# Kernel optimization log

Hardware: AMD Instinct MI355X
Metric: run time of the kernel (lower is better)

Reference implementation:

```python
import jax, jax.numpy as jnp
from jax import lax
import numpy as np

B, N = 8, 16384
C = 16            # layer_channels
K = 2             # kernel_size
L = 30            # layer_nums (layer 0 is plain causal conv, 29 gated layers)
AGG = 64          # agregate1x1 out channels
OUT = 256         # output1x1 out channels (8-bit classes)


def causal_conv(x, w, dilation):
    # x: (B, Cin, N), w: (Cout, Cin, K) -> (B, Cout, N), left-padded (causal)
    k = w.shape[-1]
    return lax.conv_general_dilated(
        x, w, window_strides=(1,), padding=[(dilation * (k - 1), 0)],
        rhs_dilation=(dilation,), dimension_numbers=('NCH', 'OIH', 'NCH'))


def setup_inputs() -> dict:
    key = jax.random.key(0)
    ks = jax.random.split(key, 16)
    s = 0.1
    x = jax.random.normal(ks[0], (B, N), dtype=jnp.float32) * 8000.0  # raw 16-bit-ish audio
    lengths = jax.random.randint(ks[1], (B,), N // 2, N, dtype=jnp.int32)
    return {
        'x': x,
        'lengths': lengths,
        'W0': jax.random.normal(ks[2], (C, 1, K), dtype=jnp.float32) * s,
        'b0': jnp.zeros((C,), dtype=jnp.float32),
        'Wf': jax.random.normal(ks[3], (L - 1, C, C, K), dtype=jnp.float32) * s,
        'bf': jnp.zeros((L - 1, C), dtype=jnp.float32),
        'Wg': jax.random.normal(ks[4], (L - 1, C, C, K), dtype=jnp.float32) * s,
        'bg': jnp.zeros((L - 1, C), dtype=jnp.float32),
        'Wr': jax.random.normal(ks[5], (L - 1, C, C), dtype=jnp.float32) * s,
        'br': jnp.zeros((L - 1, C), dtype=jnp.float32),
        'Wa': jax.random.normal(ks[6], (AGG, C), dtype=jnp.float32) * s,
        'ba': jnp.zeros((AGG,), dtype=jnp.float32),
        'Wo': jax.random.normal(ks[7], (OUT, AGG), dtype=jnp.float32) * s,
        'bo': jnp.zeros((OUT,), dtype=jnp.float32),
    }


def reference(x, lengths, W0, b0, Wf, bf, Wg, bg, Wr, br, Wa, ba, Wo, bo):
    inp = (x / 32768.0)[:, None, :]                     # (B,1,N), 65536/2 scaling
    # layer 0: plain causal conv 1 -> C
    h = causal_conv(inp, W0, 1) + b0[:, None]           # (B,C,N)
    skip = h
    inp = inp + h                                       # (B,1,N)+(B,C,N) broadcast
    for i in range(1, L):
        d = 2 ** (i % 10)
        j = i - 1
        f = jnp.tanh(causal_conv(inp, Wf[j], d) + bf[j][:, None])
        g = jax.nn.sigmoid(causal_conv(inp, Wg[j], d) + bg[j][:, None])
        z = f * g                                       # gated activation
        out = jnp.einsum('oc,bcn->bon', Wr[j], z) + br[j][:, None]
        skip = skip + out                               # skip-sum accumulation
        inp = inp + out                                 # residual
    a = jnp.einsum('oc,bcn->bon', Wa, jax.nn.relu(skip)) + ba[:, None]
    o = jnp.einsum('oc,bcn->bon', Wo, jax.nn.relu(a)) + bo[:, None]
    logp = jax.nn.log_softmax(o, axis=1)                # (B,OUT,N)
    mask = (jnp.arange(N) < lengths[:, None])[:, None, :].astype(logp.dtype)
    return logp * mask
```

## Files before the change

kernel.cpp:

```cpp
#include <hip/hip_runtime.h>
#include <hip/hip_bf16.h>

#define NN 16384
#define NC 16
#define NPOSTOT 131072
#define NLAY 29
#define TOUT 256
#define LSTR 24

typedef float4 f4;
typedef short bf16x8 __attribute__((ext_vector_type(8)));
typedef float f32x4 __attribute__((ext_vector_type(4)));

#define OFF_WF 0
#define OFF_WG (NLAY * 512)
#define OFF_WR (2 * NLAY * 512)
#define OFF_WA (3 * NLAY * 512)
#define OFF_WO (3 * NLAY * 512 + 2048)
#define PK_TOT (OFF_WO + 16384)

static __device__ __forceinline__ short to_bf16(float f) {
    __hip_bfloat16 h = __float2bfloat16(f);
    short s;
    __builtin_memcpy(&s, &h, 2);
    return s;
}
static __device__ __forceinline__ float from_bf16(short s) {
    unsigned int u = ((unsigned int)(unsigned short)s) << 16;
    float f;
    __builtin_memcpy(&f, &u, 4);
    return f;
}

__global__ __launch_bounds__(256) void prepack_k(
    const float* __restrict__ Wf, const float* __restrict__ Wg,
    const float* __restrict__ Wr, const float* __restrict__ Wa,
    const float* __restrict__ Wo, short* __restrict__ pk)
{
    const int i = blockIdx.x * 256 + threadIdx.x;
    if (i >= PK_TOT) return;
    float val;
    if (i < OFF_WG) {
        const int j = i >> 9, r = i & 511, l = r >> 3, j8 = r & 7;
        const int o = l & 15, h = l >> 4;
        const int k = h * 8 + j8, tap = k >> 4, c = k & 15;
        val = Wf[((j * 16 + o) * 16 + c) * 2 + tap];
    } else if (i < OFF_WA) {
        const int i2 = i - OFF_WG;
        if (i2 < NLAY * 512) {
            const int j = i2 >> 9, r = i2 & 511, l = r >> 3, j8 = r & 7;
            const int o = l & 15, h = l >> 4;
            const int k = h * 8 + j8, tap = k >> 4, c = k & 15;
            val = Wg[((j * 16 + o) * 16 + c) * 2 + tap];
        } else {
            const int i3 = i2 - NLAY * 512;
            const int j = i3 >> 9, r = i3 & 511, l = r >> 3, j8 = r & 7;
            const int o = l & 15, h = l >> 4;
            val = (j8 < 4) ? Wr[j * 256 + o * 16 + h * 4 + j8] : 0.0f;
        }
    } else if (i < OFF_WO) {
        const int i2 = i - OFF_WA;
        const int mt = i2 >> 9, r = i2 & 511, l = r >> 3, j8 = r & 7;
        const int og = mt * 16 + (l & 15), h = l >> 4;
        const int k = h * 8 + j8;
        val = (k < 16) ? Wa[og * 16 + k] : 0.0f;
    } else {
        const int i2 = i - OFF_WO;
        const int qt = i2 >> 10, hf = (i2 >> 9) & 1, r = i2 & 511;
        const int l = r >> 3, j8 = r & 7;
        const int q = qt * 16 + (l & 15), h = l >> 4;
        const int kg = hf * 32 + (j8 >> 2) * 16 + h * 4 + (j8 & 3);
        val = Wo[q * 64 + kg];
    }
    pk[i] = to_bf16(val);
}

static __device__ __forceinline__ f32x4 gated_core2(
    bf16x8 bx, bf16x8 af_, bf16x8 ag_, bf16x8 ar_,
    f32x4 cf, f32x4 cg, f32x4 cr)
{
    const f32x4 fp = __builtin_amdgcn_mfma_f32_16x16x32_bf16(af_, bx, cf, 0, 0, 0);
    const f32x4 gp = __builtin_amdgcn_mfma_f32_16x16x32_bf16(ag_, bx, cg, 0, 0, 0);

    bf16x8 bz;
#pragma unroll
    for (int r = 0; r < 4; ++r) {
        const float ef = __expf(2.0f * fminf(fp[r], 43.0f));
        const float eg = __expf(-gp[r]);
        const float den = fmaf(ef, eg, ef) + (eg + 1.0f);
        bz[r] = to_bf16((ef - 1.0f) * __builtin_amdgcn_rcpf(den));
        bz[r + 4] = 0;
    }
    return __builtin_amdgcn_mfma_f32_16x16x32_bf16(ar_, bx = bz, cr, 0, 0, 0);
}

struct SegCfg { int d[8]; int nl; int jbase; int H; int l0; };

constexpr SegCfg CFGS[12] = {
    {{2, 4, 8, 16, 32, 64, 0, 0},  6, 0,  128, 1},
    {{128, 0, 0, 0, 0, 0, 0, 0},   1, 6,  0,   0},
    {{256, 0, 0, 0, 0, 0, 0, 0},   1, 7,  0,   0},
    {{512, 1, 2, 4, 8, 16, 32, 0}, 7, 8,  64,  0},
    {{64, 0, 0, 0, 0, 0, 0, 0},    1, 15, 0,   0},
    {{128, 0, 0, 0, 0, 0, 0, 0},   1, 16, 0,   0},
    {{256, 0, 0, 0, 0, 0, 0, 0},   1, 17, 0,   0},
    {{512, 1, 2, 4, 8, 16, 32, 0}, 7, 18, 64,  0},
    {{64, 0, 0, 0, 0, 0, 0, 0},    1, 25, 0,   0},
    {{128, 0, 0, 0, 0, 0, 0, 0},   1, 26, 0,   0},
    {{256, 0, 0, 0, 0, 0, 0, 0},   1, 27, 0,   0},
    {{512, 0, 0, 0, 0, 0, 0, 0},   1, 28, 0,   0},
};

template<int KI>
__global__ __launch_bounds__((TOUT + CFGS[KI].H) * 2)
void fused_t(const short* __restrict__ src, const float* __restrict__ x,
             const float* __restrict__ W0, const float* __restrict__ b0,
             short* __restrict__ dst, const short* __restrict__ pk,
             const float* __restrict__ bfA, const float* __restrict__ bgA,
             const float* __restrict__ brA)
{
    constexpr SegCfg cfg = CFGS[KI];
    constexpr int H = cfg.H;
    constexpr int Wp = TOUT + H;
    constexpr bool MULTI = (cfg.nl > 1);
    constexpr int LDSSZ = MULTI ? 2 * Wp * LSTR : 8;
    __shared__ short lds[LDSSZ];
    short* ldsA = lds;
    short* ldsB = lds + (MULTI ? Wp * LSTR : 0);

    const int t = threadIdx.x, lane = t & 63, wv = t >> 6;
    const int h = lane >> 4, i16 = lane & 15;
    const int tap = h >> 1, c0 = (h & 1) * 8;
    const int pbase = blockIdx.x * TOUT;
    const int bb = pbase >> 14, n0 = pbase & (NN - 1);
    const float* xrow = x + (size_t)bb * NN;
    const short* srow = src + (size_t)bb * NN * NC;

    const int l0r = wv * 32 + i16;
    const int l1r = l0r + 16;
    const int nA = n0 - H + l0r;
    const int nB = nA + 16;

    f32x4 res0, res1;

    {
        constexpr int d = cfg.d[0];
        constexpr int j = cfg.jbase;
        const bf16x8 af = *(const bf16x8*)(pk + OFF_WF + j * 512 + lane * 8);
        const bf16x8 ag = *(const bf16x8*)(pk + OFF_WG + j * 512 + lane * 8);
        const bf16x8 ar = *(const bf16x8*)(pk + OFF_WR + j * 512 + lane * 8);
        const f4 v1 = *(const f4*)(bfA + j * 16 + h * 4);
        const f4 v2 = *(const f4*)(bgA + j * 16 + h * 4);
        const f4 v3 = *(const f4*)(brA + j * 16 + h * 4);
        const f32x4 cf = {v1.x, v1.y, v1.z, v1.w};
        const f32x4 cg = {v2.x, v2.y, v2.z, v2.w};
        const f32x4 cr = {v3.x, v3.y, v3.z, v3.w};

        auto tile0 = [&](int l, int n, f32x4& res) {
            const int ns = tap ? n : n - d;
            bf16x8 bx = {0, 0, 0, 0, 0, 0, 0, 0};
            if (cfg.l0) {
                if (ns >= 0) {
                    const float xs = xrow[ns] * (1.0f / 32768.0f);
                    const float xm = (ns >= 1) ? xrow[ns - 1] * (1.0f / 32768.0f) : 0.0f;
#pragma unroll
                    for (int q2 = 0; q2 < 8; ++q2) {
                        const int c = c0 + q2;
                        bx[q2] = to_bf16(xs + fmaf(W0[c * 2], xm,
                                          fmaf(W0[c * 2 + 1], xs, b0[c])));
                    }
                }
            } else {
                if (ns >= 0) bx = *(const bf16x8*)(srow + (size_t)ns * NC + c0);
            }
            const f32x4 o = gated_core2(bx, af, ag, ar, cf, cg, cr);

            float r0, r1, r2, r3;
            if (cfg.l0) {
                if (n >= 0) {
                    const float xs = xrow[n] * (1.0f / 32768.0f);
                    const float xm = (n >= 1) ? xrow[n - 1] * (1.0f / 32768.0f) : 0.0f;
                    const int c = h * 4;
                    r0 = xs + fmaf(W0[c * 2 + 0], xm, fmaf(W0[c * 2 + 1], xs, b0[c + 0]));
                    r1 = xs + fmaf(W0[c * 2 + 2], xm, fmaf(W0[c * 2 + 3], xs, b0[c + 1]));
                    r2 = xs + fmaf(W0[c * 2 + 4], xm, fmaf(W0[c * 2 + 5], xs, b0[c + 2]));
                    r3 = xs + fmaf(W0[c * 2 + 6], xm, fmaf(W0[c * 2 + 7], xs, b0[c + 3]));
                } else { r0 = r1 = r2 = r3 = 0.0f; }
            } else {
                if (n >= 0) {
                    const short4 ov = *(const short4*)(srow + (size_t)n * NC + h * 4);
                    r0 = from_bf16(ov.x); r1 = from_bf16(ov.y);
                    r2 = from_bf16(ov.z); r3 = from_bf16(ov.w);
                } else { r0 = r1 = r2 = r3 = 0.0f; }
            }
            res[0] = r0 + o[0]; res[1] = r1 + o[1];
            res[2] = r2 + o[2]; res[3] = r3 + o[3];
            if (MULTI) {
                *(short4*)(ldsA + l * LSTR + h * 4) =
                    make_short4(to_bf16(res[0]), to_bf16(res[1]),
                                to_bf16(res[2]), to_bf16(res[3]));
            }
        };
        tile0(l0r, nA, res0);
        tile0(l1r, nB, res1);
    }
    if (MULTI) __syncthreads();

    int cur = 0;
#pragma unroll
    for (int s = 1; s < cfg.nl; ++s) {
        const int d = cfg.d[s];
        const int j = cfg.jbase + s;
        const bf16x8 af = *(const bf16x8*)(pk + OFF_WF + j * 512 + lane * 8);
        const bf16x8 ag = *(const bf16x8*)(pk + OFF_WG + j * 512 + lane * 8);
        const bf16x8 ar = *(const bf16x8*)(pk + OFF_WR + j * 512 + lane * 8);
        const f4 v1 = *(const f4*)(bfA + j * 16 + h * 4);
        const f4 v2 = *(const f4*)(bgA + j * 16 + h * 4);
        const f4 v3 = *(const f4*)(brA + j * 16 + h * 4);
        const f32x4 cf = {v1.x, v1.y, v1.z, v1.w};
        const f32x4 cg = {v2.x, v2.y, v2.z, v2.w};
        const f32x4 cr = {v3.x, v3.y, v3.z, v3.w};
        const short* rb = cur ? ldsB : ldsA;
        short* wb = cur ? ldsA : ldsB;
        const bool wr = (s + 1 < cfg.nl);

        auto tileL = [&](int l, int n, f32x4& res) {
            const int nt = tap ? n : n - d;
            int lt = tap ? l : l - d;
            if (lt < 0) lt = 0;
            bf16x8 bx = {0, 0, 0, 0, 0, 0, 0, 0};
            if (nt >= 0) bx = *(const bf16x8*)(rb + lt * LSTR + c0);
            const f32x4 o = gated_core2(bx, af, ag, ar, cf, cg, cr);
            res[0] += o[0]; res[1] += o[1]; res[2] += o[2]; res[3] += o[3];
            if (wr) {
                *(short4*)(wb + l * LSTR + h * 4) =
                    make_short4(to_bf16(res[0]), to_bf16(res[1]),
                                to_bf16(res[2]), to_bf16(res[3]));
            }
        };
        tileL(l0r, nA, res0);
        tileL(l1r, nB, res1);
        if (s + 1 < cfg.nl) __syncthreads();
        cur ^= 1;
    }

    if (l0r >= H) {
        *(short4*)(dst + ((size_t)bb * NN + nA) * NC + h * 4) =
            make_short4(to_bf16(res0[0]), to_bf16(res0[1]),
                        to_bf16(res0[2]), to_bf16(res0[3]));
    }
    if (l1r >= H) {
        *(short4*)(dst + ((size_t)bb * NN + nB) * NC + h * 4) =
            make_short4(to_bf16(res1[0]), to_bf16(res1[1]),
                        to_bf16(res1[2]), to_bf16(res1[3]));
    }
}

__global__ __launch_bounds__(512, 2) void headm_k(
    const short* __restrict__ fin, const float* __restrict__ x,
    const int* __restrict__ lengths,
    const short* __restrict__ pka, const float* __restrict__ ba,
    const short* __restrict__ pko, const float* __restrict__ bo,
    float* __restrict__ out)
{
    __shared__ short ldsW[16384];

    const int t = threadIdx.x;
    const int lane = t & 63;
    const int wv = t >> 6;
    const int i16 = lane & 15;
    const int h = lane >> 4;
    const int pos = blockIdx.x * 128 + wv * 16 + i16;
    const int b = pos >> 14;
    const int n = pos & (NN - 1);

#pragma unroll
    for (int i = 0; i < 4; ++i)
        ((f4*)ldsW)[t + i * 512] = ((const f4*)pko)[t + i * 512];

    bf16x8 bs;
    if (h < 2) {
        const float xs = x[pos] * (1.0f / 32768.0f);
        const bf16x8 v = *(const bf16x8*)(fin + (size_t)pos * NC + h * 8);
#pragma unroll
        for (int j = 0; j < 8; ++j)
            bs[j] = to_bf16(fmaxf(from_bf16(v[j]) - xs, 0.0f));
    } else {
#pragma unroll
        for (int j = 0; j < 8; ++j) bs[j] = 0;
    }

    float ra[16];
#pragma unroll
    for (int mt = 0; mt < 4; ++mt) {
        const bf16x8 aa = *(const bf16x8*)(pka + (mt * 64 + lane) * 8);
        const f4 bav = *(const f4*)(ba + mt * 16 + h * 4);
        f32x4 c = {bav.x, bav.y, bav.z, bav.w};
        c = __builtin_amdgcn_mfma_f32_16x16x32_bf16(aa, bs, c, 0, 0, 0);
#pragma unroll
        for (int r = 0; r < 4; ++r) ra[mt * 4 + r] = fmaxf(c[r], 0.0f);
    }
    bf16x8 blo, bhi;
#pragma unroll
    for (int j = 0; j < 8; ++j) { blo[j] = to_bf16(ra[j]); bhi[j] = to_bf16(ra[8 + j]); }

    __syncthreads();

    float lg[64];
#pragma unroll
    for (int qt = 0; qt < 16; ++qt) {
        const bf16x8 a0 = *(const bf16x8*)(ldsW + ((qt * 2 + 0) * 64 + lane) * 8);
        const bf16x8 a1 = *(const bf16x8*)(ldsW + ((qt * 2 + 1) * 64 + lane) * 8);
        const f4 bov = *(const f4*)(bo + qt * 16 + h * 4);
        f32x4 c = {bov.x, bov.y, bov.z, bov.w};
        c = __builtin_amdgcn_mfma_f32_16x16x32_bf16(a0, blo, c, 0, 0, 0);
        c = __builtin_amdgcn_mfma_f32_16x16x32_bf16(a1, bhi, c, 0, 0, 0);
#pragma unroll
        for (int r = 0; r < 4; ++r) lg[qt * 4 + r] = c[r];
    }

    float m = lg[0];
#pragma unroll
    for (int j = 1; j < 64; ++j) m = fmaxf(m, lg[j]);
    m = fmaxf(m, __shfl_xor(m, 16, 64));
    m = fmaxf(m, __shfl_xor(m, 32, 64));
    float s = 0.0f;
#pragma unroll
    for (int j = 0; j < 64; ++j) s += __expf(lg[j] - m);
    s += __shfl_xor(s, 16, 64);
    s += __shfl_xor(s, 32, 64);
    const float lse = m + __logf(s);
    const bool valid = n < lengths[b];

    float* ob = out + (size_t)b * 256 * NN + n;
#pragma unroll
    for (int qt = 0; qt < 16; ++qt)
#pragma unroll
        for (int r = 0; r < 4; ++r)
            ob[(size_t)(qt * 16 + h * 4 + r) * NN] = valid ? (lg[qt * 4 + r] - lse) : 0.0f;
}

extern "C" void kernel_launch(void* const* d_in, const int* in_sizes, int n_in,
                              void* d_out, int out_size, void* d_ws, size_t ws_size,
                              hipStream_t stream)
{
    const float* x       = (const float*)d_in[0];
    const int*   lengths = (const int*)d_in[1];
    const float* W0      = (const float*)d_in[2];
    const float* b0      = (const float*)d_in[3];
    const float* Wf      = (const float*)d_in[4];
    const float* bf      = (const float*)d_in[5];
    const float* Wg      = (const float*)d_in[6];
    const float* bg      = (const float*)d_in[7];
    const float* Wr      = (const float*)d_in[8];
    const float* br      = (const float*)d_in[9];
    const float* Wa      = (const float*)d_in[10];
    const float* ba      = (const float*)d_in[11];
    const float* Wo      = (const float*)d_in[12];
    const float* bo      = (const float*)d_in[13];
    float* out = (float*)d_out;

    short* bufA = (short*)d_ws;
    short* bufB = bufA + (size_t)NPOSTOT * NC;
    short* pk   = bufB + (size_t)NPOSTOT * NC;

    prepack_k<<<dim3((PK_TOT + 255) / 256), dim3(256), 0, stream>>>(
        Wf, Wg, Wr, Wa, Wo, pk);

#define FUSED(K, SRC, DST)                                                     \
    fused_t<K><<<dim3(NPOSTOT / TOUT), dim3((TOUT + CFGS[K].H) * 2), 0,        \
                 stream>>>(SRC, x, W0, b0, DST, pk, bf, bg, br)

    FUSED(0,  bufA, bufA);
    FUSED(1,  bufA, bufB);
    FUSED(2,  bufB, bufA);
    FUSED(3,  bufA, bufB);
    FUSED(4,  bufB, bufA);
    FUSED(5,  bufA, bufB);
    FUSED(6,  bufB, bufA);
    FUSED(7,  bufA, bufB);
    FUSED(8,  bufB, bufA);
    FUSED(9,  bufA, bufB);
    FUSED(10, bufB, bufA);
    FUSED(11, bufA, bufB);
#undef FUSED

    headm_k<<<dim3(NPOSTOT / 128), dim3(512), 0, stream>>>(
        bufB, x, lengths, pk + OFF_WA, ba, pk + OFF_WO, bo, out);
}
```

Measured before the change: 143.1 us.

## Switch gated layers to 32x32x16 MFMA with fused filter/gate tile

Replaces the three 16x16x32 MFMAs per tile (filter, gate, residual) with 32x32x16 MFMAs. Filter and gate weights are stacked into one 32-row A matrix, the two taps are split across two MFMAs, and channels are permuted so the accumulator layout lines up with the B operand of the next layer. Each lane now keeps 8 channels of the residual in registers and reuses them as the tap-0 input instead of reloading from LDS. Block size and output tile are retuned per segment: multi-layer segments use 128 outputs and non-multi segments 256. This is meant to cut MFMA count and wasted zero-padding work, at the cost of a more intricate weight-prepack permutation and different occupancy.

```diff
diff --git a/kernel.cpp b/kernel.cpp
--- a/kernel.cpp
+++ b/kernel.cpp
@@ -5,19 +5,22 @@
 #define NC 16
 #define NPOSTOT 131072
 #define NLAY 29
-#define TOUT 256
 #define LSTR 24
 
 typedef float4 f4;
 typedef short bf16x8 __attribute__((ext_vector_type(8)));
 typedef float f32x4 __attribute__((ext_vector_type(4)));
-
-#define OFF_WF 0
-#define OFF_WG (NLAY * 512)
-#define OFF_WR (2 * NLAY * 512)
-#define OFF_WA (3 * NLAY * 512)
-#define OFF_WO (3 * NLAY * 512 + 2048)
+typedef float f32x16 __attribute__((ext_vector_type(16)));
+
+#define OFF_C  0
+#define OFF_R  (NLAY * 1024)
+#define OFF_WA (OFF_R + NLAY * 512)
+#define OFF_WO (OFF_WA + 2048)
 #define PK_TOT (OFF_WO + 16384)
+
+__host__ __device__ constexpr int PERM(int s) {
+    return (s & 3) | ((s & 4) << 1) | ((s & 8) >> 1);
+}
 
 static __device__ __forceinline__ short to_bf16(float f) {
     __hip_bfloat16 h = __float2bfloat16(f);
@@ -40,34 +43,28 @@
     const int i = blockIdx.x * 256 + threadIdx.x;
     if (i >= PK_TOT) return;
     float val;
-    if (i < OFF_WG) {
-        const int j = i >> 9, r = i & 511, l = r >> 3, j8 = r & 7;
-        const int o = l & 15, h = l >> 4;
-        const int k = h * 8 + j8, tap = k >> 4, c = k & 15;
-        val = Wf[((j * 16 + o) * 16 + c) * 2 + tap];
+    if (i < OFF_R) {
+        const int j = i >> 10, r = i & 1023, tp = r >> 9, rr = r & 511;
+        const int l = rr >> 3, j8 = rr & 7;
+        const int row = l & 31, hi = l >> 5;
+        const int c = PERM(hi * 8 + j8);
+        val = (row < 16) ? Wf[((j * 16 + row) * 16 + c) * 2 + tp]
+                         : Wg[((j * 16 + (row - 16)) * 16 + c) * 2 + tp];
     } else if (i < OFF_WA) {
-        const int i2 = i - OFF_WG;
-        if (i2 < NLAY * 512) {
-            const int j = i2 >> 9, r = i2 & 511, l = r >> 3, j8 = r & 7;
-            const int o = l & 15, h = l >> 4;
-            const int k = h * 8 + j8, tap = k >> 4, c = k & 15;
-            val = Wg[((j * 16 + o) * 16 + c) * 2 + tap];
-        } else {
-            const int i3 = i2 - NLAY * 512;
-            const int j = i3 >> 9, r = i3 & 511, l = r >> 3, j8 = r & 7;
-            const int o = l & 15, h = l >> 4;
-            val = (j8 < 4) ? Wr[j * 256 + o * 16 + h * 4 + j8] : 0.0f;
-        }
+        const int i2 = i - OFF_R;
+        const int j = i2 >> 9, rr = i2 & 511, l = rr >> 3, j8 = rr & 7;
+        const int row = l & 31, hi = l >> 5;
+        val = (row < 16) ? Wr[j * 256 + row * 16 + PERM(hi * 8 + j8)] : 0.0f;
     } else if (i < OFF_WO) {
         const int i2 = i - OFF_WA;
-        const int mt = i2 >> 9, r = i2 & 511, l = r >> 3, j8 = r & 7;
+        const int mt = i2 >> 9, rr = i2 & 511, l = rr >> 3, j8 = rr & 7;
         const int og = mt * 16 + (l & 15), h = l >> 4;
         const int k = h * 8 + j8;
-        val = (k < 16) ? Wa[og * 16 + k] : 0.0f;
+        val = (k < 16) ? Wa[og * 16 + PERM(k)] : 0.0f;
     } else {
         const int i2 = i - OFF_WO;
-        const int qt = i2 >> 10, hf = (i2 >> 9) & 1, r = i2 & 511;
-        const int l = r >> 3, j8 = r & 7;
+        const int qt = i2 >> 10, hf = (i2 >> 9) & 1, rr = i2 & 511;
+        const int l = rr >> 3, j8 = rr & 7;
         const int q = qt * 16 + (l & 15), h = l >> 4;
         const int kg = hf * 32 + (j8 >> 2) * 16 + h * 4 + (j8 & 3);
         val = Wo[q * 64 + kg];
@@ -75,44 +72,65 @@
     pk[i] = to_bf16(val);
 }
 
-static __device__ __forceinline__ f32x4 gated_core2(
-    bf16x8 bx, bf16x8 af_, bf16x8 ag_, bf16x8 ar_,
-    f32x4 cf, f32x4 cg, f32x4 cr)
-{
-    const f32x4 fp = __builtin_amdgcn_mfma_f32_16x16x32_bf16(af_, bx, cf, 0, 0, 0);
-    const f32x4 gp = __builtin_amdgcn_mfma_f32_16x16x32_bf16(ag_, bx, cg, 0, 0, 0);
+static __device__ __forceinline__ void layer32(
+    bf16x8 b0v, bf16x8 b1v, const short* __restrict__ pk, int j,
+    const float* __restrict__ bfA, const float* __restrict__ bgA,
+    const float* __restrict__ brA, int lane, int hi4,
+    float* res, bf16x8& cur)
+{
+    const bf16x8 a0 = *(const bf16x8*)(pk + OFF_C + j * 1024 + lane * 8);
+    const bf16x8 a1 = *(const bf16x8*)(pk + OFF_C + j * 1024 + 512 + lane * 8);
+    const bf16x8 ar = *(const bf16x8*)(pk + OFF_R + j * 512 + lane * 8);
+    const f4 bf0 = *(const f4*)(bfA + j * 16 + hi4);
+    const f4 bf1 = *(const f4*)(bfA + j * 16 + 8 + hi4);
+    const f4 bg0 = *(const f4*)(bgA + j * 16 + hi4);
+    const f4 bg1 = *(const f4*)(bgA + j * 16 + 8 + hi4);
+
+    f32x16 acc = {bf0.x, bf0.y, bf0.z, bf0.w, bf1.x, bf1.y, bf1.z, bf1.w,
+                  bg0.x, bg0.y, bg0.z, bg0.w, bg1.x, bg1.y, bg1.z, bg1.w};
+    acc = __builtin_amdgcn_mfma_f32_32x32x16_bf16(a0, b0v, acc, 0, 0, 0);
+    acc = __builtin_amdgcn_mfma_f32_32x32x16_bf16(a1, b1v, acc, 0, 0, 0);
 
     bf16x8 bz;
 #pragma unroll
-    for (int r = 0; r < 4; ++r) {
-        const float ef = __expf(2.0f * fminf(fp[r], 43.0f));
-        const float eg = __expf(-gp[r]);
+    for (int r = 0; r < 8; ++r) {
+        const float ef = __expf(2.0f * fminf(acc[r], 43.0f));
+        const float eg = __expf(-acc[r + 8]);
         const float den = fmaf(ef, eg, ef) + (eg + 1.0f);
         bz[r] = to_bf16((ef - 1.0f) * __builtin_amdgcn_rcpf(den));
-        bz[r + 4] = 0;
-    }
-    return __builtin_amdgcn_mfma_f32_16x16x32_bf16(ar_, bx = bz, cr, 0, 0, 0);
-}
-
-struct SegCfg { int d[8]; int nl; int jbase; int H; int l0; };
+    }
+
+    const f4 br0 = *(const f4*)(brA + j * 16 + hi4);
+    const f4 br1 = *(const f4*)(brA + j * 16 + 8 + hi4);
+    f32x16 cr = {br0.x, br0.y, br0.z, br0.w, br1.x, br1.y, br1.z, br1.w,
+                 0.0f, 0.0f, 0.0f, 0.0f, 0.0f, 0.0f, 0.0f, 0.0f};
+    const f32x16 o = __builtin_amdgcn_mfma_f32_32x32x16_bf16(ar, bz, cr, 0, 0, 0);
+
+#pragma unroll
+    for (int r = 0; r < 8; ++r) res[r] += o[r];
+#pragma unroll
+    for (int r = 0; r < 8; ++r) cur[r] = to_bf16(res[r]);
+}
+
+struct SegCfg { int d[8]; int nl; int jbase; int H; int l0; int tout; };
 
 constexpr SegCfg CFGS[12] = {
-    {{2, 4, 8, 16, 32, 64, 0, 0},  6, 0,  128, 1},
-    {{128, 0, 0, 0, 0, 0, 0, 0},   1, 6,  0,   0},
-    {{256, 0, 0, 0, 0, 0, 0, 0},   1, 7,  0,   0},
-    {{512, 1, 2, 4, 8, 16, 32, 0}, 7, 8,  64,  0},
-    {{64, 0, 0, 0, 0, 0, 0, 0},    1, 15, 0,   0},
-    {{128, 0, 0, 0, 0, 0, 0, 0},   1, 16, 0,   0},
-    {{256, 0, 0, 0, 0, 0, 0, 0},   1, 17, 0,   0},
-    {{512, 1, 2, 4, 8, 16, 32, 0}, 7, 18, 64,  0},
-    {{64, 0, 0, 0, 0, 0, 0, 0},    1, 25, 0,   0},
-    {{128, 0, 0, 0, 0, 0, 0, 0},   1, 26, 0,   0},
-    {{256, 0, 0, 0, 0, 0, 0, 0},   1, 27, 0,   0},
-    {{512, 0, 0, 0, 0, 0, 0, 0},   1, 28, 0,   0},
+    {{2, 4, 8, 16, 32, 64, 0, 0},  6, 0,  128, 1, 128},
+    {{128, 0, 0, 0, 0, 0, 0, 0},   1, 6,  0,   0, 256},
+    {{256, 0, 0, 0, 0, 0, 0, 0},   1, 7,  0,   0, 256},
+    {{512, 1, 2, 4, 8, 16, 32, 0}, 7, 8,  64,  0, 128},
+    {{64, 0, 0, 0, 0, 0, 0, 0},    1, 15, 0,   0, 256},
+    {{128, 0, 0, 0, 0, 0, 0, 0},   1, 16, 0,   0, 256},
+    {{256, 0, 0, 0, 0, 0, 0, 0},   1, 17, 0,   0, 256},
+    {{512, 1, 2, 4, 8, 16, 32, 0}, 7, 18, 64,  0, 128},
+    {{64, 0, 0, 0, 0, 0, 0, 0},    1, 25, 0,   0, 256},
+    {{128, 0, 0, 0, 0, 0, 0, 0},   1, 26, 0,   0, 256},
+    {{256, 0, 0, 0, 0, 0, 0, 0},   1, 27, 0,   0, 256},
+    {{512, 0, 0, 0, 0, 0, 0, 0},   1, 28, 0,   0, 256},
 };
 
 template<int KI>
-__global__ __launch_bounds__((TOUT + CFGS[KI].H) * 2)
+__global__ __launch_bounds__(CFGS[KI].tout + CFGS[KI].H)
 void fused_t(const short* __restrict__ src, const float* __restrict__ x,
              const float* __restrict__ W0, const float* __restrict__ b0,
              short* __restrict__ dst, const short* __restrict__ pk,
@@ -121,7 +139,9 @@
 {
     constexpr SegCfg cfg = CFGS[KI];
     constexpr int H = cfg.H;
+    constexpr int TOUT = cfg.tout;
     constexpr int Wp = TOUT + H;
+    constexpr int W = Wp / 64;
     constexpr bool MULTI = (cfg.nl > 1);
     constexpr int LDSSZ = MULTI ? 2 * Wp * LSTR : 8;
     __shared__ short lds[LDSSZ];
@@ -129,131 +149,95 @@
     short* ldsB = lds + (MULTI ? Wp * LSTR : 0);
 
     const int t = threadIdx.x, lane = t & 63, wv = t >> 6;
-    const int h = lane >> 4, i16 = lane & 15;
-    const int tap = h >> 1, c0 = (h & 1) * 8;
+    const int hi = lane >> 5, hi4 = hi * 4, s0 = hi * 8;
+    const int p31 = lane & 31;
     const int pbase = blockIdx.x * TOUT;
     const int bb = pbase >> 14, n0 = pbase & (NN - 1);
     const float* xrow = x + (size_t)bb * NN;
     const short* srow = src + (size_t)bb * NN * NC;
 
-    const int l0r = wv * 32 + i16;
-    const int l1r = l0r + 16;
+    const int l0r = wv * 32 + p31;
+    const int l1r = l0r + W * 32;
     const int nA = n0 - H + l0r;
-    const int nB = nA + 16;
-
-    f32x4 res0, res1;
+    const int nB = n0 - H + l1r;
+
+    float res0[8], res1[8];
+    bf16x8 cur0, cur1;
 
     {
         constexpr int d = cfg.d[0];
         constexpr int j = cfg.jbase;
-        const bf16x8 af = *(const bf16x8*)(pk + OFF_WF + j * 512 + lane * 8);
-        const bf16x8 ag = *(const bf16x8*)(pk + OFF_WG + j * 512 + lane * 8);
-        const bf16x8 ar = *(const bf16x8*)(pk + OFF_WR + j * 512 + lane * 8);
-        const f4 v1 = *(const f4*)(bfA + j * 16 + h * 4);
-        const f4 v2 = *(const f4*)(bgA + j * 16 + h * 4);
-        const f4 v3 = *(const f4*)(brA + j * 16 + h * 4);
-        const f32x4 cf = {v1.x, v1.y, v1.z, v1.w};
-        const f32x4 cg = {v2.x, v2.y, v2.z, v2.w};
-        const f32x4 cr = {v3.x, v3.y, v3.z, v3.w};
-
-        auto tile0 = [&](int l, int n, f32x4& res) {
-            const int ns = tap ? n : n - d;
-            bf16x8 bx = {0, 0, 0, 0, 0, 0, 0, 0};
+        auto tile0 = [&](int l, int n, float* res, bf16x8& cur) {
+            const int ns = n - d;
+            bf16x8 b0v = {0, 0, 0, 0, 0, 0, 0, 0};
+            bf16x8 b1v = {0, 0, 0, 0, 0, 0, 0, 0};
             if (cfg.l0) {
                 if (ns >= 0) {
                     const float xs = xrow[ns] * (1.0f / 32768.0f);
                     const float xm = (ns >= 1) ? xrow[ns - 1] * (1.0f / 32768.0f) : 0.0f;
 #pragma unroll
-                    for (int q2 = 0; q2 < 8; ++q2) {
-                        const int c = c0 + q2;
-                        bx[q2] = to_bf16(xs + fmaf(W0[c * 2], xm,
+                    for (int q = 0; q < 8; ++q) {
+                        const int c = PERM(s0 + q);
+                        b0v[q] = to_bf16(xs + fmaf(W0[c * 2], xm,
                                           fmaf(W0[c * 2 + 1], xs, b0[c])));
                     }
                 }
-            } else {
-                if (ns >= 0) bx = *(const bf16x8*)(srow + (size_t)ns * NC + c0);
-            }
-            const f32x4 o = gated_core2(bx, af, ag, ar, cf, cg, cr);
-
-            float r0, r1, r2, r3;
-            if (cfg.l0) {
                 if (n >= 0) {
                     const float xs = xrow[n] * (1.0f / 32768.0f);
                     const float xm = (n >= 1) ? xrow[n - 1] * (1.0f / 32768.0f) : 0.0f;
-                    const int c = h * 4;
-                    r0 = xs + fmaf(W0[c * 2 + 0], xm, fmaf(W0[c * 2 + 1], xs, b0[c + 0]));
-                    r1 = xs + fmaf(W0[c * 2 + 2], xm, fmaf(W0[c * 2 + 3], xs, b0[c + 1]));
-                    r2 = xs + fmaf(W0[c * 2 + 4], xm, fmaf(W0[c * 2 + 5], xs, b0[c + 2]));
-                    r3 = xs + fmaf(W0[c * 2 + 6], xm, fmaf(W0[c * 2 + 7], xs, b0[c + 3]));
-                } else { r0 = r1 = r2 = r3 = 0.0f; }
+#pragma unroll
+                    for (int q = 0; q < 8; ++q) {
+                        const int c = PERM(s0 + q);
+                        res[q] = xs + fmaf(W0[c * 2], xm,
+                                  fmaf(W0[c * 2 + 1], xs, b0[c]));
+                        b1v[q] = to_bf16(res[q]);
+                    }
+                } else {
+#pragma unroll
+                    for (int q = 0; q < 8; ++q) res[q] = 0.0f;
+                }
             } else {
-                if (n >= 0) {
-                    const short4 ov = *(const short4*)(srow + (size_t)n * NC + h * 4);
-                    r0 = from_bf16(ov.x); r1 = from_bf16(ov.y);
-                    r2 = from_bf16(ov.z); r3 = from_bf16(ov.w);
-                } else { r0 = r1 = r2 = r3 = 0.0f; }
+                if (ns >= 0) b0v = *(const bf16x8*)(srow + (size_t)ns * NC + s0);
+                if (n >= 0)  b1v = *(const bf16x8*)(srow + (size_t)n * NC + s0);
+#pragma unroll
+                for (int q = 0; q < 8; ++q) res[q] = from_bf16(b1v[q]);
             }
-            res[0] = r0 + o[0]; res[1] = r1 + o[1];
-            res[2] = r2 + o[2]; res[3] = r3 + o[3];
-            if (MULTI) {
-                *(short4*)(ldsA + l * LSTR + h * 4) =
-                    make_short4(to_bf16(res[0]), to_bf16(res[1]),
-                                to_bf16(res[2]), to_bf16(res[3]));
-            }
+            layer32(b0v, b1v, pk, j, bfA, bgA, brA, lane, hi4, res, cur);
+            if (MULTI) *(bf16x8*)(ldsA + l * LSTR + s0) = cur;
         };
-        tile0(l0r, nA, res0);
-        tile0(l1r, nB, res1);
+        tile0(l0r, nA, res0, cur0);
+        tile0(l1r, nB, res1, cur1);
     }
     if (MULTI) __syncthreads();
 
-    int cur = 0;
+    int curb = 0;
 #pragma unroll
     for (int s = 1; s < cfg.nl; ++s) {
         const int d = cfg.d[s];
         const int j = cfg.jbase + s;
-        const bf16x8 af = *(const bf16x8*)(pk + OFF_WF + j * 512 + lane * 8);
-        const bf16x8 ag = *(const bf16x8*)(pk + OFF_WG + j * 512 + lane * 8);
-        const bf16x8 ar = *(const bf16x8*)(pk + OFF_WR + j * 512 + lane * 8);
-        const f4 v1 = *(const f4*)(bfA + j * 16 + h * 4);
-        const f4 v2 = *(const f4*)(bgA + j * 16 + h * 4);
-        const f4 v3 = *(const f4*)(brA + j * 16 + h * 4);
-        const f32x4 cf = {v1.x, v1.y, v1.z, v1.w};
-        const f32x4 cg = {v2.x, v2.y, v2.z, v2.w};
-        const f32x4 cr = {v3.x, v3.y, v3.z, v3.w};
-        const short* rb = cur ? ldsB : ldsA;
-        short* wb = cur ? ldsA : ldsB;
+        const short* rb = curb ? ldsB : ldsA;
+        short* wb = curb ? ldsA : ldsB;
         const bool wr = (s + 1 < cfg.nl);
 
-        auto tileL = [&](int l, int n, f32x4& res) {
-            const int nt = tap ? n : n - d;
-            int lt = tap ? l : l - d;
+        auto tileL = [&](int l, int n, float* res, bf16x8& cur) {
+            const int nt = n - d;
+            int lt = l - d;
             if (lt < 0) lt = 0;
-            bf16x8 bx = {0, 0, 0, 0, 0, 0, 0, 0};
-            if (nt >= 0) bx = *(const bf16x8*)(rb + lt * LSTR + c0);
-            const f32x4 o = gated_core2(bx, af, ag, ar, cf, cg, cr);
-            res[0] += o[0]; res[1] += o[1]; res[2] += o[2]; res[3] += o[3];
-            if (wr) {
-                *(short4*)(wb + l * LSTR + h * 4) =
-                    make_short4(to_bf16(res[0]), to_bf16(res[1]),
-                                to_bf16(res[2]), to_bf16(res[3]));
-            }
+            bf16x8 b0v = {0, 0, 0, 0, 0, 0, 0, 0};
+            if (nt >= 0) b0v = *(const bf16x8*)(rb + lt * LSTR + s0);
+            layer32(b0v, cur, pk, j, bfA, bgA, brA, lane, hi4, res, cur);
+            if (wr) *(bf16x8*)(wb + l * LSTR + s0) = cur;
         };
-        tileL(l0r, nA, res0);
-        tileL(l1r, nB, res1);
-        if (s + 1 < cfg.nl) __syncthreads();
-        cur ^= 1;
-    }
-
-    if (l0r >= H) {
-        *(short4*)(dst + ((size_t)bb * NN + nA) * NC + h * 4) =
-            make_short4(to_bf16(res0[0]), to_bf16(res0[1]),
-                        to_bf16(res0[2]), to_bf16(res0[3]));
-    }
-    if (l1r >= H) {
-        *(short4*)(dst + ((size_t)bb * NN + nB) * NC + h * 4) =
-            make_short4(to_bf16(res1[0]), to_bf16(res1[1]),
-                        to_bf16(res1[2]), to_bf16(res1[3]));
-    }
+        tileL(l0r, nA, res0, cur0);
+        tileL(l1r, nB, res1, cur1);
+        if (wr) __syncthreads();
+        curb ^= 1;
+    }
+
+    if (l0r >= H)
+        *(bf16x8*)(dst + ((size_t)bb * NN + nA) * NC + s0) = cur0;
+    if (l1r >= H)
+        *(bf16x8*)(dst + ((size_t)bb * NN + nB) * NC + s0) = cur1;
 }
 
 __global__ __launch_bounds__(512, 2) void headm_k(
@@ -368,8 +352,9 @@
         Wf, Wg, Wr, Wa, Wo, pk);
 
 #define FUSED(K, SRC, DST)                                                     \
-    fused_t<K><<<dim3(NPOSTOT / TOUT), dim3((TOUT + CFGS[K].H) * 2), 0,        \
-                 stream>>>(SRC, x, W0, b0, DST, pk, bf, bg, br)
+    fused_t<K><<<dim3(NPOSTOT / CFGS[K].tout),                                 \
+                 dim3(CFGS[K].tout + CFGS[K].H), 0, stream>>>(                 \
+        SRC, x, W0, b0, DST, pk, bf, bg, br)
 
     FUSED(0,  bufA, bufA);
     FUSED(1,  bufA, bufB);
```

After: 164.7 us. 15.1% more time.

## Split multi-layer fused segments into one kernel launch per layer

Applied to the files above, without the earlier changes.

Replaces the segmented kernels, which chained several dilated layers through double-buffered LDS with halo recomputation, with one kernel per gated layer (29 launches). Each launch reads its input and residual straight from the global buffer and writes the updated residual back. This removes halo recompute, LDS traffic and block-wide barriers. In exchange it adds launches and a full global read/write of the activation buffer for every layer. The head now reads from the other ping-pong buffer to match the new layer count.

```diff
diff --git a/kernel.cpp b/kernel.cpp
--- a/kernel.cpp
+++ b/kernel.cpp
@@ -6,7 +6,6 @@
 #define NPOSTOT 131072
 #define NLAY 29
 #define TOUT 256
-#define LSTR 24
 
 typedef float4 f4;
 typedef short bf16x8 __attribute__((ext_vector_type(8)));
@@ -91,28 +90,22 @@
         bz[r] = to_bf16((ef - 1.0f) * __builtin_amdgcn_rcpf(den));
         bz[r + 4] = 0;
     }
-    return __builtin_amdgcn_mfma_f32_16x16x32_bf16(ar_, bx = bz, cr, 0, 0, 0);
-}
-
-struct SegCfg { int d[8]; int nl; int jbase; int H; int l0; };
-
-constexpr SegCfg CFGS[12] = {
-    {{2, 4, 8, 16, 32, 64, 0, 0},  6, 0,  128, 1},
-    {{128, 0, 0, 0, 0, 0, 0, 0},   1, 6,  0,   0},
-    {{256, 0, 0, 0, 0, 0, 0, 0},   1, 7,  0,   0},
-    {{512, 1, 2, 4, 8, 16, 32, 0}, 7, 8,  64,  0},
-    {{64, 0, 0, 0, 0, 0, 0, 0},    1, 15, 0,   0},
-    {{128, 0, 0, 0, 0, 0, 0, 0},   1, 16, 0,   0},
-    {{256, 0, 0, 0, 0, 0, 0, 0},   1, 17, 0,   0},
-    {{512, 1, 2, 4, 8, 16, 32, 0}, 7, 18, 64,  0},
-    {{64, 0, 0, 0, 0, 0, 0, 0},    1, 25, 0,   0},
-    {{128, 0, 0, 0, 0, 0, 0, 0},   1, 26, 0,   0},
-    {{256, 0, 0, 0, 0, 0, 0, 0},   1, 27, 0,   0},
-    {{512, 0, 0, 0, 0, 0, 0, 0},   1, 28, 0,   0},
+    return __builtin_amdgcn_mfma_f32_16x16x32_bf16(ar_, bz, cr, 0, 0, 0);
+}
+
+struct SegCfg { int d; int jbase; int l0; };
+
+constexpr SegCfg CFGS[NLAY] = {
+    {2, 0, 1},   {4, 1, 0},   {8, 2, 0},   {16, 3, 0},  {32, 4, 0},
+    {64, 5, 0},  {128, 6, 0}, {256, 7, 0}, {512, 8, 0}, {1, 9, 0},
+    {2, 10, 0},  {4, 11, 0},  {8, 12, 0},  {16, 13, 0}, {32, 14, 0},
+    {64, 15, 0}, {128, 16, 0},{256, 17, 0},{512, 18, 0},{1, 19, 0},
+    {2, 20, 0},  {4, 21, 0},  {8, 22, 0},  {16, 23, 0}, {32, 24, 0},
+    {64, 25, 0}, {128, 26, 0},{256, 27, 0},{512, 28, 0},
 };
 
 template<int KI>
-__global__ __launch_bounds__((TOUT + CFGS[KI].H) * 2)
+__global__ __launch_bounds__(512)
 void fused_t(const short* __restrict__ src, const float* __restrict__ x,
              const float* __restrict__ W0, const float* __restrict__ b0,
              short* __restrict__ dst, const short* __restrict__ pk,
@@ -120,13 +113,8 @@
              const float* __restrict__ brA)
 {
     constexpr SegCfg cfg = CFGS[KI];
-    constexpr int H = cfg.H;
-    constexpr int Wp = TOUT + H;
-    constexpr bool MULTI = (cfg.nl > 1);
-    constexpr int LDSSZ = MULTI ? 2 * Wp * LSTR : 8;
-    __shared__ short lds[LDSSZ];
-    short* ldsA = lds;
-    short* ldsB = lds + (MULTI ? Wp * LSTR : 0);
+    constexpr int d = cfg.d;
+    constexpr int j = cfg.jbase;
 
     const int t = threadIdx.x, lane = t & 63, wv = t >> 6;
     const int h = lane >> 4, i16 = lane & 15;
@@ -136,124 +124,57 @@
     const float* xrow = x + (size_t)bb * NN;
     const short* srow = src + (size_t)bb * NN * NC;
 
+    const bf16x8 af = *(const bf16x8*)(pk + OFF_WF + j * 512 + lane * 8);
+    const bf16x8 ag = *(const bf16x8*)(pk + OFF_WG + j * 512 + lane * 8);
+    const bf16x8 ar = *(const bf16x8*)(pk + OFF_WR + j * 512 + lane * 8);
+    const f4 v1 = *(const f4*)(bfA + j * 16 + h * 4);
+    const f4 v2 = *(const f4*)(bgA + j * 16 + h * 4);
+    const f4 v3 = *(const f4*)(brA + j * 16 + h * 4);
+    const f32x4 cf = {v1.x, v1.y, v1.z, v1.w};
+    const f32x4 cg = {v2.x, v2.y, v2.z, v2.w};
+    const f32x4 cr = {v3.x, v3.y, v3.z, v3.w};
+
     const int l0r = wv * 32 + i16;
-    const int l1r = l0r + 16;
-    const int nA = n0 - H + l0r;
+    const int nA = n0 + l0r;
     const int nB = nA + 16;
 
-    f32x4 res0, res1;
-
-    {
-        constexpr int d = cfg.d[0];
-        constexpr int j = cfg.jbase;
-        const bf16x8 af = *(const bf16x8*)(pk + OFF_WF + j * 512 + lane * 8);
-        const bf16x8 ag = *(const bf16x8*)(pk + OFF_WG + j * 512 + lane * 8);
-        const bf16x8 ar = *(const bf16x8*)(pk + OFF_WR + j * 512 + lane * 8);
-        const f4 v1 = *(const f4*)(bfA + j * 16 + h * 4);
-        const f4 v2 = *(const f4*)(bgA + j * 16 + h * 4);
-        const f4 v3 = *(const f4*)(brA + j * 16 + h * 4);
-        const f32x4 cf = {v1.x, v1.y, v1.z, v1.w};
-        const f32x4 cg = {v2.x, v2.y, v2.z, v2.w};
-        const f32x4 cr = {v3.x, v3.y, v3.z, v3.w};
-
-        auto tile0 = [&](int l, int n, f32x4& res) {
-            const int ns = tap ? n : n - d;
-            bf16x8 bx = {0, 0, 0, 0, 0, 0, 0, 0};
-            if (cfg.l0) {
-                if (ns >= 0) {
-                    const float xs = xrow[ns] * (1.0f / 32768.0f);
-                    const float xm = (ns >= 1) ? xrow[ns - 1] * (1.0f / 32768.0f) : 0.0f;
-#pragma unroll
-                    for (int q2 = 0; q2 < 8; ++q2) {
-                        const int c = c0 + q2;
-                        bx[q2] = to_bf16(xs + fmaf(W0[c * 2], xm,
-                                          fmaf(W0[c * 2 + 1], xs, b0[c])));
-                    }
+    auto doTile = [&](int n) {
+        const int ns = tap ? n : n - d;
+        bf16x8 bx = {0, 0, 0, 0, 0, 0, 0, 0};
+        f32x4 rin = {0.0f, 0.0f, 0.0f, 0.0f};
+        if (cfg.l0) {
+            if (ns >= 0) {
+                const float xs = xrow[ns] * (1.0f / 32768.0f);
+                const float xm = (ns >= 1) ? xrow[ns - 1] * (1.0f / 32768.0f) : 0.0f;
+#pragma unroll
+                for (int q2 = 0; q2 < 8; ++q2) {
+                    const int c = c0 + q2;
+                    bx[q2] = to_bf16(xs + fmaf(W0[c * 2], xm,
+                                      fmaf(W0[c * 2 + 1], xs, b0[c])));
                 }
-            } else {
-                if (ns >= 0) bx = *(const bf16x8*)(srow + (size_t)ns * NC + c0);
             }
-            const f32x4 o = gated_core2(bx, af, ag, ar, cf, cg, cr);
-
-            float r0, r1, r2, r3;
-            if (cfg.l0) {
-                if (n >= 0) {
-                    const float xs = xrow[n] * (1.0f / 32768.0f);
-                    const float xm = (n >= 1) ? xrow[n - 1] * (1.0f / 32768.0f) : 0.0f;
-                    const int c = h * 4;
-                    r0 = xs + fmaf(W0[c * 2 + 0], xm, fmaf(W0[c * 2 + 1], xs, b0[c + 0]));
-                    r1 = xs + fmaf(W0[c * 2 + 2], xm, fmaf(W0[c * 2 + 3], xs, b0[c + 1]));
-                    r2 = xs + fmaf(W0[c * 2 + 4], xm, fmaf(W0[c * 2 + 5], xs, b0[c + 2]));
-                    r3 = xs + fmaf(W0[c * 2 + 6], xm, fmaf(W0[c * 2 + 7], xs, b0[c + 3]));
-                } else { r0 = r1 = r2 = r3 = 0.0f; }
-            } else {
-                if (n >= 0) {
-                    const short4 ov = *(const short4*)(srow + (size_t)n * NC + h * 4);
-                    r0 = from_bf16(ov.x); r1 = from_bf16(ov.y);
-                    r2 = from_bf16(ov.z); r3 = from_bf16(ov.w);
-                } else { r0 = r1 = r2 = r3 = 0.0f; }
+            {
+                const float xs = xrow[n] * (1.0f / 32768.0f);
+                const float xm = (n >= 1) ? xrow[n - 1] * (1.0f / 32768.0f) : 0.0f;
+                const int c = h * 4;
+                rin[0] = xs + fmaf(W0[c * 2 + 0], xm, fmaf(W0[c * 2 + 1], xs, b0[c + 0]));
+                rin[1] = xs + fmaf(W0[c * 2 + 2], xm, fmaf(W0[c * 2 + 3], xs, b0[c + 1]));
+                rin[2] = xs + fmaf(W0[c * 2 + 4], xm, fmaf(W0[c * 2 + 5], xs, b0[c + 2]));
+                rin[3] = xs + fmaf(W0[c * 2 + 6], xm, fmaf(W0[c * 2 + 7], xs, b0[c + 3]));
             }
-            res[0] = r0 + o[0]; res[1] = r1 + o[1];
-            res[2] = r2 + o[2]; res[3] = r3 + o[3];
-            if (MULTI) {
-                *(short4*)(ldsA + l * LSTR + h * 4) =
-                    make_short4(to_bf16(res[0]), to_bf16(res[1]),
-                                to_bf16(res[2]), to_bf16(res[3]));
-            }
-        };
-        tile0(l0r, nA, res0);
-        tile0(l1r, nB, res1);
-    }
-    if (MULTI) __syncthreads();
-
-    int cur = 0;
-#pragma unroll
-    for (int s = 1; s < cfg.nl; ++s) {
-        const int d = cfg.d[s];
-        const int j = cfg.jbase + s;
-        const bf16x8 af = *(const bf16x8*)(pk + OFF_WF + j * 512 + lane * 8);
-        const bf16x8 ag = *(const bf16x8*)(pk + OFF_WG + j * 512 + lane * 8);
-        const bf16x8 ar = *(const bf16x8*)(pk + OFF_WR + j * 512 + lane * 8);
-        const f4 v1 = *(const f4*)(bfA + j * 16 + h * 4);
-        const f4 v2 = *(const f4*)(bgA + j * 16 + h * 4);
-        const f4 v3 = *(const f4*)(brA + j * 16 + h * 4);
-        const f32x4 cf = {v1.x, v1.y, v1.z, v1.w};
-        const f32x4 cg = {v2.x, v2.y, v2.z, v2.w};
-        const f32x4 cr = {v3.x, v3.y, v3.z, v3.w};
-        const short* rb = cur ? ldsB : ldsA;
-        short* wb = cur ? ldsA : ldsB;
-        const bool wr = (s + 1 < cfg.nl);
-
-        auto tileL = [&](int l, int n, f32x4& res) {
-            const int nt = tap ? n : n - d;
-            int lt = tap ? l : l - d;
-            if (lt < 0) lt = 0;
-            bf16x8 bx = {0, 0, 0, 0, 0, 0, 0, 0};
-            if (nt >= 0) bx = *(const bf16x8*)(rb + lt * LSTR + c0);
-            const f32x4 o = gated_core2(bx, af, ag, ar, cf, cg, cr);
-            res[0] += o[0]; res[1] += o[1]; res[2] += o[2]; res[3] += o[3];
-            if (wr) {
-                *(short4*)(wb + l * LSTR + h * 4) =
-                    make_short4(to_bf16(res[0]), to_bf16(res[1]),
-                                to_bf16(res[2]), to_bf16(res[3]));
-            }
-        };
-        tileL(l0r, nA, res0);
-        tileL(l1r, nB, res1);
-        if (s + 1 < cfg.nl) __syncthreads();
-        cur ^= 1;
-    }
-
-    if (l0r >= H) {
-        *(short4*)(dst + ((size_t)bb * NN + nA) * NC + h * 4) =
-            make_short4(to_bf16(res0[0]), to_bf16(res0[1]),
-                        to_bf16(res0[2]), to_bf16(res0[3]));
-    }
-    if (l1r >= H) {
-        *(short4*)(dst + ((size_t)bb * NN + nB) * NC + h * 4) =
-            make_short4(to_bf16(res1[0]), to_bf16(res1[1]),
-                        to_bf16(res1[2]), to_bf16(res1[3]));
-    }
+        } else {
+            if (ns >= 0) bx = *(const bf16x8*)(srow + (size_t)ns * NC + c0);
+            const short4 ov = *(const short4*)(srow + (size_t)n * NC + h * 4);
+            rin[0] = from_bf16(ov.x); rin[1] = from_bf16(ov.y);
+            rin[2] = from_bf16(ov.z); rin[3] = from_bf16(ov.w);
+        }
+        const f32x4 o = gated_core2(bx, af, ag, ar, cf, cg, cr);
+        *(short4*)(dst + ((size_t)bb * NN + n) * NC + h * 4) =
+            make_short4(to_bf16(rin[0] + o[0]), to_bf16(rin[1] + o[1]),
+                        to_bf16(rin[2] + o[2]), to_bf16(rin[3] + o[3]));
+    };
+    doTile(nA);
+    doTile(nB);
 }
 
 __global__ __launch_bounds__(512, 2) void headm_k(
@@ -368,8 +289,8 @@
         Wf, Wg, Wr, Wa, Wo, pk);
 
 #define FUSED(K, SRC, DST)                                                     \
-    fused_t<K><<<dim3(NPOSTOT / TOUT), dim3((TOUT + CFGS[K].H) * 2), 0,        \
-                 stream>>>(SRC, x, W0, b0, DST, pk, bf, bg, br)
+    fused_t<K><<<dim3(NPOSTOT / TOUT), dim3(512), 0, stream>>>(                \
+        SRC, x, W0, b0, DST, pk, bf, bg, br)
 
     FUSED(0,  bufA, bufA);
     FUSED(1,  bufA, bufB);
@@ -383,8 +304,25 @@
     FUSED(9,  bufA, bufB);
     FUSED(10, bufB, bufA);
     FUSED(11, bufA, bufB);
+    FUSED(12, bufB, bufA);
+    FUSED(13, bufA, bufB);
+    FUSED(14, bufB, bufA);
+    FUSED(15, bufA, bufB);
+    FUSED(16, bufB, bufA);
+    FUSED(17, bufA, bufB);
+    FUSED(18, bufB, bufA);
+    FUSED(19, bufA, bufB);
+    FUSED(20, bufB, bufA);
+    FUSED(21, bufA, bufB);
+    FUSED(22, bufB, bufA);
+    FUSED(23, bufA, bufB);
+    FUSED(24, bufB, bufA);
+    FUSED(25, bufA, bufB);
+    FUSED(26, bufB, bufA);
+    FUSED(27, bufA, bufB);
+    FUSED(28, bufB, bufA);
 #undef FUSED
 
     headm_k<<<dim3(NPOSTOT / 128), dim3(512), 0, stream>>>(
-        bufB, x, lengths, pk + OFF_WA, ba, pk + OFF_WO, bo, out);
-}
+        bufA, x, lengths, pk + OFF_WA, ba, pk + OFF_WO, bo, out);
+}
```

Result: slower. 172.0 us (+20.2%).
